# Performance work log

Measured on AMD Instinct MI355X. Metric: run time of the kernel, lower is better.

## Reference

```python
import jax, jax.numpy as jnp
import numpy as np

GROUPS = 32
EPS = 1e-5


def setup_inputs() -> dict:
    key = jax.random.key(0)
    ks = jax.random.split(key, 6)
    B, H, W, C = 2, 64, 64, 512
    wscale = 0.02  # keep logits in a sane range for softmax
    return {
        "x": jax.random.normal(ks[0], (B, H, W, C), dtype=jnp.float32),
        "gamma": jnp.ones((C,), jnp.float32),
        "beta": jnp.zeros((C,), jnp.float32),
        "wq": jax.random.normal(ks[1], (C, C), dtype=jnp.float32) * wscale,
        "bq": jnp.zeros((C,), jnp.float32),
        "wk": jax.random.normal(ks[2], (C, C), dtype=jnp.float32) * wscale,
        "bk": jnp.zeros((C,), jnp.float32),
        "wv": jax.random.normal(ks[3], (C, C), dtype=jnp.float32) * wscale,
        "bv": jnp.zeros((C,), jnp.float32),
        "wp": jax.random.normal(ks[4], (C, C), dtype=jnp.float32) * wscale,
        "bp": jnp.zeros((C,), jnp.float32),
    }


def _group_norm(x, gamma, beta):
    B, H, W, C = x.shape
    xg = x.reshape(B, H, W, GROUPS, C // GROUPS)
    mean = xg.mean(axis=(1, 2, 4), keepdims=True)
    var = xg.var(axis=(1, 2, 4), keepdims=True)
    xn = ((xg - mean) * jax.lax.rsqrt(var + EPS)).reshape(B, H, W, C)
    return xn * gamma + beta


def reference(x, gamma, beta, wq, bq, wk, bk, wv, bv, wp, bp):
    B, H, W, C = x.shape
    xn = _group_norm(x, gamma, beta)
    # 1x1 convs == per-pixel linear layers
    q = (xn @ wq + bq).reshape(B, H * W, C)
    k = (xn @ wk + bk).reshape(B, H * W, C)
    v = (xn @ wv + bv).reshape(B, H * W, C)
    scale = C ** (-0.5)
    attn = jax.nn.softmax(jnp.einsum("bqc,bkc->bqk", q, k) * scale, axis=-1)
    out = jnp.einsum("bqk,bkc->bqc", attn, v).reshape(B, H, W, C)
    return (out @ wp + bp) + x
```

## Files before the change

kernel.cpp:

```cpp
#include <hip/hip_runtime.h>


typedef __bf16 bf16_t;
typedef __bf16 bf16x8 __attribute__((ext_vector_type(8)));
typedef __bf16 bf16x4 __attribute__((ext_vector_type(4)));
typedef float  f32x4  __attribute__((ext_vector_type(4)));

__device__ __forceinline__ bf16x8 ld8(const bf16_t* p) {
    return *reinterpret_cast<const bf16x8*>(p);
}
__device__ __forceinline__ f32x4 mfma16(bf16x8 a, bf16x8 b, f32x4 c) {
    return __builtin_amdgcn_mfma_f32_16x16x32_bf16(a, b, c, 0, 0, 0);
}
__device__ __forceinline__ void gload16(const bf16_t* gp, bf16_t* lp) {
    __builtin_amdgcn_global_load_lds(
        (const __attribute__((address_space(1))) void*)gp,
        (__attribute__((address_space(3))) void*)lp, 16, 0, 0);
}

#define NPIX 8192
#define C512 512
#define SEQ  4096
#define QSCALE 0.044194173824159216f

__global__ __launch_bounds__(256) void gn_sum_k(const float* __restrict__ x,
                                                float* __restrict__ accum) {
    int bg    = blockIdx.x >> 3;
    int slice = blockIdx.x & 7;
    int b = bg >> 5, g = bg & 31;
    const float* xp = x + (size_t)b * SEQ * C512 + g * 16;
    float s = 0.f, s2 = 0.f;
    #pragma unroll
    for (int pp = 0; pp < 2; pp++) {
        int p = slice * 512 + pp * 256 + threadIdx.x;
        const float4* q = reinterpret_cast<const float4*>(xp + (size_t)p * C512);
        #pragma unroll
        for (int i = 0; i < 4; i++) {
            float4 v = q[i];
            s  += v.x + v.y + v.z + v.w;
            s2 += v.x*v.x + v.y*v.y + v.z*v.z + v.w*v.w;
        }
    }
    #pragma unroll
    for (int off = 32; off >= 1; off >>= 1) {
        s  += __shfl_down(s, off);
        s2 += __shfl_down(s2, off);
    }
    __shared__ float rs[4], rs2[4];
    int wave = threadIdx.x >> 6;
    if ((threadIdx.x & 63) == 0) { rs[wave] = s; rs2[wave] = s2; }
    __syncthreads();
    if (threadIdx.x == 0) {
        float S = rs[0] + rs[1] + rs[2] + rs[3];
        float S2 = rs2[0] + rs2[1] + rs2[2] + rs2[3];
        atomicAdd(&accum[bg * 2],     S);
        atomicAdd(&accum[bg * 2 + 1], S2);
    }
}

__global__ __launch_bounds__(256) void wt_conv_k(const float* wq, const float* wk,
                                                 const float* wv, const float* wp,
                                                 bf16_t* wqkvT, bf16_t* wpT) {
    int y = blockIdx.y;
    const float* w = (y == 0) ? wq : (y == 1) ? wk : (y == 2) ? wv : wp;
    float scale = (y == 0) ? QSCALE : 1.0f;
    int tid = blockIdx.x * 256 + threadIdx.x;
    int n = tid >> 9, k = tid & 511;
    bf16_t val = (bf16_t)(w[(size_t)k * C512 + n] * scale);
    if (y < 3) wqkvT[((size_t)y * C512 + n) * C512 + k] = val;
    else       wpT[(size_t)n * C512 + k] = val;
}

__global__ __launch_bounds__(256) void bias_merge_k(const float* bq, const float* bk,
                                                    const float* bv, float* bqkv) {
    int i = blockIdx.x * 256 + threadIdx.x;
    float v = (i < 512) ? bq[i] * QSCALE : (i < 1024) ? bk[i - 512] : bv[i - 1024];
    bqkv[i] = v;
}

__global__ __launch_bounds__(256) void xn_k(const float* __restrict__ x,
                                            const float* __restrict__ accum,
                                            const float* __restrict__ gamma,
                                            const float* __restrict__ beta,
                                            bf16_t* __restrict__ xn) {
    size_t idx = ((size_t)blockIdx.x * 256 + threadIdx.x) * 4;
    int c = (int)(idx & 511);
    size_t pix = idx >> 9;
    int b = (int)(pix >> 12);
    int g = c >> 4;
    float sum = accum[(b * 32 + g) * 2];
    float ssq = accum[(b * 32 + g) * 2 + 1];
    float mean = sum * (1.f / 65536.f);
    float var  = ssq * (1.f / 65536.f) - mean * mean;
    float rstd = rsqrtf(var + 1e-5f);
    float4 v  = *reinterpret_cast<const float4*>(x + idx);
    float4 gm = *reinterpret_cast<const float4*>(gamma + c);
    float4 bt = *reinterpret_cast<const float4*>(beta + c);
    bf16x4 o;
    o[0] = (bf16_t)((v.x - mean) * rstd * gm.x + bt.x);
    o[1] = (bf16_t)((v.y - mean) * rstd * gm.y + bt.y);
    o[2] = (bf16_t)((v.z - mean) * rstd * gm.z + bt.z);
    o[3] = (bf16_t)((v.w - mean) * rstd * gm.w + bt.w);
    *reinterpret_cast<bf16x4*>(xn + idx) = o;
}

template <int MODE>
__global__ __launch_bounds__(256, 2) void gemm128_k(
        const bf16_t* __restrict__ Aall, const bf16_t* __restrict__ Ball,
        const float* __restrict__ bias, const float* __restrict__ resid,
        void* __restrict__ out0, void* __restrict__ out1,
        void* __restrict__ out2, void* __restrict__ out3,
        float* __restrict__ lsum) {
    constexpr int TM  = (MODE == 3) ? 64 : 128;
    constexpr int ASZ = TM * 32;
    constexpr int ACH = TM / 16;
    constexpr int CPW = (ACH + 8) / 4;
    constexpr int MI  = TM / 32;
    __shared__ bf16_t smem[2 * ASZ + 8192];

    int lane = threadIdx.x & 63;
    int w    = threadIdx.x >> 6;
    int wr   = w >> 1, wc = w & 1;
    int lrow = lane & 15, quad = lane >> 4;

    const bf16_t* A = Aall;
    const bf16_t* B = Ball;
    size_t lda = 512, ldb = 512;
    int ksteps = 16;

    int bm = blockIdx.x * TM, bn = blockIdx.y * 128;

    auto stage = [&](int buf, int ks) {
        size_t k0 = (size_t)ks * 32;
        #pragma unroll
        for (int ii = 0; ii < CPW; ii++) {
            int c = w * CPW + ii;
            if (c < ACH) {
                const bf16_t* gpA = A + (size_t)(bm + c * 16 + lrow) * lda + k0 + quad * 8;
                gload16(gpA, &smem[buf * ASZ + c * 512]);
            } else {
                int cb = c - ACH;
                const bf16_t* gpB = B + (size_t)(bn + cb * 16 + lrow) * ldb + k0 + quad * 8;
                gload16(gpB, &smem[2 * ASZ + buf * 4096 + cb * 512]);
            }
        }
    };

    f32x4 acc[MI][4] = {};

    stage(0, 0);

    for (int ks = 0; ks < ksteps; ks++) {
        int cur = ks & 1;
        __syncthreads();
        if (ks + 1 < ksteps) stage(1 - cur, ks + 1);

        const bf16_t* al = &smem[cur * ASZ + (wr * MI) * 512];
        const bf16_t* bl = &smem[2 * ASZ + cur * 4096 + (wc * 4) * 512];
        bf16x8 af[MI], bf[4];
        #pragma unroll
        for (int m = 0; m < MI; m++) af[m] = ld8(al + m * 512 + lane * 8);
        #pragma unroll
        for (int n = 0; n < 4; n++) bf[n] = ld8(bl + n * 512 + lane * 8);
        #pragma unroll
        for (int m = 0; m < MI; m++)
            #pragma unroll
            for (int n = 0; n < 4; n++)
                acc[m][n] = mfma16(af[m], bf[n], acc[m][n]);
    }

    #pragma unroll
    for (int m = 0; m < MI; m++) {
        int rowb = bm + wr * (TM / 2) + m * 16 + quad * 4;
        #pragma unroll
        for (int n = 0; n < 4; n++) {
            int col = bn + wc * 64 + n * 16 + lrow;
            #pragma unroll
            for (int i = 0; i < 4; i++) {
                int row = rowb + i;
                float v = acc[m][n][i];
                if (MODE == 0) {
                    int seg = col >> 9, c = col & 511;
                    bf16_t val = (bf16_t)(v + bias[col]);
                    if (seg == 0) {
                        ((bf16_t*)out0)[(size_t)row * C512 + c] = val;
                    } else if (seg == 1) {
                        ((bf16_t*)out1)[(size_t)row * C512 + c] = val;
                    } else {
                        int b = row >> 12, s = row & 4095;
                        ((bf16_t*)out2)[((size_t)(b * C512 + c)) * SEQ + s] = val;
                    }
                } else {
                    size_t idx = (size_t)row * C512 + col;
                    ((float*)out0)[idx] = v + bias[col] + resid[idx];
                }
            }
        }
    }
}

__global__ __launch_bounds__(512, 1) void fattn_k(
        const bf16_t* __restrict__ Q, const bf16_t* __restrict__ K,
        const bf16_t* __restrict__ VT, bf16_t* __restrict__ Op0,
        bf16_t* __restrict__ Op1, float* __restrict__ lsum) {
    __shared__ bf16_t Kl[2][32 * 512];
    __shared__ bf16_t Vl[2][512 * 32];
    __shared__ bf16_t Pl[64 * 32];

    int bid = blockIdx.x;
    int xcd = bid & 7, loc = bid >> 3;
    int b   = (xcd >> 1) & 1;
    int kv  = xcd & 1;
    int q0  = ((xcd >> 2) * 32 + loc) * 64;
    int key0 = kv * 2048;

    const bf16_t* Qb = Q  + (size_t)b * SEQ * C512;
    const bf16_t* Kb = K  + (size_t)b * SEQ * C512;
    const bf16_t* Vb = VT + (size_t)b * C512 * SEQ;
    bf16_t* Op = kv ? Op1 : Op0;

    int lane = threadIdx.x & 63;
    int w    = threadIdx.x >> 6;
    int lrow = lane & 15, quad = lane >> 4;
    int qt = w & 3, kt = w >> 2;

    bf16x8 qf[16];
    const bf16_t* qp = Qb + (size_t)(q0 + qt * 16 + lrow) * C512 + quad * 8;
    #pragma unroll
    for (int ks = 0; ks < 16; ks++) qf[ks] = ld8(qp + ks * 32);

    auto stage = [&](int buf, int t) {
        #pragma unroll
        for (int ii = 0; ii < 8; ii++) {
            int cc = w * 8 + ii;
            if (cc < 32) {
                int ks = cc >> 1, ktc = cc & 1;
                const bf16_t* gp = Kb +
                    (size_t)(key0 + t * 32 + ktc * 16 + lrow) * C512 + ks * 32 + quad * 8;
                gload16(gp, &Kl[buf][cc * 512]);
            } else {
                int ct = cc - 32;
                const bf16_t* gp = Vb +
                    (size_t)(ct * 16 + lrow) * SEQ + key0 + t * 32 + quad * 8;
                gload16(gp, &Vl[buf][ct * 512]);
            }
        }
    };

    f32x4 oacc[4][4] = {};
    float rs[4] = {0.f, 0.f, 0.f, 0.f};

    stage(0, 0);

    for (int t = 0; t < 64; t++) {
        int cur = t & 1;
        __syncthreads();
        if (t < 63) stage(cur ^ 1, t + 1);

        f32x4 sa = {0.f, 0.f, 0.f, 0.f};
        #pragma unroll
        for (int ks = 0; ks < 16; ks++) {
            bf16x8 bf = ld8(&Kl[cur][(ks * 2 + kt) * 512 + lane * 8]);
            sa = mfma16(qf[ks], bf, sa);
        }
        #pragma unroll
        for (int i = 0; i < 4; i++) {
            float p = __expf(fminf(sa[i], 20.0f));
            rs[i] += p;
            int off = qt * 512 + (quad * 4 + i) * 8 +
                      (kt * 2 + (lrow >> 3)) * 128 + (lrow & 7);
            Pl[off] = (bf16_t)p;
        }
        asm volatile("s_waitcnt lgkmcnt(0)" ::: "memory");
        __builtin_amdgcn_s_barrier();
        __builtin_amdgcn_sched_barrier(0);

        bf16x8 pa[4];
        #pragma unroll
        for (int m = 0; m < 4; m++) pa[m] = ld8(&Pl[m * 512 + lane * 8]);
        #pragma unroll
        for (int n = 0; n < 4; n++) {
            bf16x8 vf = ld8(&Vl[cur][(w * 4 + n) * 512 + lane * 8]);
            #pragma unroll
            for (int m = 0; m < 4; m++)
                oacc[m][n] = mfma16(pa[m], vf, oacc[m][n]);
        }
    }

    #pragma unroll
    for (int i = 0; i < 4; i++) {
        float r = rs[i];
        r += __shfl_xor(r, 1);
        r += __shfl_xor(r, 2);
        r += __shfl_xor(r, 4);
        r += __shfl_xor(r, 8);
        if (lrow == 0)
            atomicAdd(&lsum[(size_t)b * SEQ + q0 + qt * 16 + quad * 4 + i], r);
    }

    #pragma unroll
    for (int m = 0; m < 4; m++) {
        int row = q0 + m * 16 + quad * 4;
        #pragma unroll
        for (int n = 0; n < 4; n++) {
            int col = w * 64 + n * 16 + lrow;
            #pragma unroll
            for (int i = 0; i < 4; i++)
                Op[((size_t)b * SEQ + row + i) * C512 + col] = (bf16_t)oacc[m][n][i];
        }
    }
}

__global__ __launch_bounds__(256) void attn_combine2_k(
        const bf16_t* __restrict__ Op0, const bf16_t* __restrict__ Op1,
        const float* __restrict__ lsum, bf16_t* __restrict__ O) {
    int idx = blockIdx.x * 256 + threadIdx.x;
    int row = idx >> 6;
    int c8  = (idx & 63) << 3;
    float inv = 1.0f / lsum[row];
    size_t base = (size_t)row * C512 + c8;
    bf16x8 o0 = ld8(Op0 + base), o1 = ld8(Op1 + base);
    bf16x8 o;
    #pragma unroll
    for (int j = 0; j < 8; j++)
        o[j] = (bf16_t)(((float)o0[j] + (float)o1[j]) * inv);
    *reinterpret_cast<bf16x8*>(O + base) = o;
}

extern "C" void kernel_launch(void* const* d_in, const int* in_sizes, int n_in,
                              void* d_out, int out_size, void* d_ws, size_t ws_size,
                              hipStream_t stream) {
    const float* x     = (const float*)d_in[0];
    const float* gamma = (const float*)d_in[1];
    const float* beta  = (const float*)d_in[2];
    const float* wq = (const float*)d_in[3];  const float* bq = (const float*)d_in[4];
    const float* wk = (const float*)d_in[5];  const float* bk = (const float*)d_in[6];
    const float* wv = (const float*)d_in[7];  const float* bv = (const float*)d_in[8];
    const float* wp = (const float*)d_in[9];  const float* bp = (const float*)d_in[10];
    float* out = (float*)d_out;

    char* ws = (char*)d_ws;
    size_t off = 0;
    float*  bqkv   = (float*)(ws + off);   off += 1536 * sizeof(float);
    float*  lsum   = (float*)(ws + off);   off += (size_t)NPIX * sizeof(float);
    float*  accum  = (float*)(ws + off);   off += 128 * sizeof(float);
    bf16_t* xn     = (bf16_t*)(ws + off);  off += (size_t)NPIX * C512 * 2;
    bf16_t* wqkvT  = (bf16_t*)(ws + off);  off += (size_t)3 * C512 * C512 * 2;
    bf16_t* wpT    = (bf16_t*)(ws + off);  off += (size_t)C512 * C512 * 2;
    bf16_t* Qb     = (bf16_t*)(ws + off);  off += (size_t)NPIX * C512 * 2;
    bf16_t* Kb     = (bf16_t*)(ws + off);  off += (size_t)NPIX * C512 * 2;
    bf16_t* VTb    = (bf16_t*)(ws + off);  off += (size_t)NPIX * C512 * 2;
    bf16_t* Op0    = (bf16_t*)(ws + off);  off += (size_t)NPIX * C512 * 2;
    bf16_t* Op1    = (bf16_t*)(ws + off);  off += (size_t)NPIX * C512 * 2;
    bf16_t* Ob  = xn;

    hipMemsetAsync(lsum, 0, (size_t)(NPIX + 128) * sizeof(float), stream);

    gn_sum_k<<<512, 256, 0, stream>>>(x, accum);
    wt_conv_k<<<dim3(1024, 4), 256, 0, stream>>>(wq, wk, wv, wp, wqkvT, wpT);
    bias_merge_k<<<6, 256, 0, stream>>>(bq, bk, bv, bqkv);
    xn_k<<<4096, 256, 0, stream>>>(x, accum, gamma, beta, xn);

    gemm128_k<0><<<dim3(64, 12, 1), 256, 0, stream>>>(
        xn, wqkvT, bqkv, nullptr, Qb, Kb, VTb, nullptr, nullptr);

    fattn_k<<<256, 512, 0, stream>>>(Qb, Kb, VTb, Op0, Op1, lsum);

    attn_combine2_k<<<2048, 256, 0, stream>>>(Op0, Op1, lsum, Ob);

    gemm128_k<3><<<dim3(128, 4, 1), 256, 0, stream>>>(
        Ob, wpT, bp, x, out, nullptr, nullptr, nullptr, nullptr);
}
```

Before: 305.3 us.

## Warp-specialize attention: QK/softmax waves feed PV waves via double-buffered P

Splits the eight waves of the flash-attention block into two roles. Four waves compute QK^T and exp for 64 queries and write P into a double-buffered LDS tile. The other four waves load V and run the PV MFMAs one key tile behind. The aim is to overlap the score phase with the value phase instead of serializing them behind a barrier on every tile. In exchange, each wave now holds more accumulator registers (32 f32x4 on the PV side), and the pipeline needs one extra iteration to drain.

```diff
diff --git a/kernel.cpp b/kernel.cpp
--- a/kernel.cpp
+++ b/kernel.cpp
@@ -204,8 +204,8 @@
         const bf16_t* __restrict__ VT, bf16_t* __restrict__ Op0,
         bf16_t* __restrict__ Op1, float* __restrict__ lsum) {
     __shared__ bf16_t Kl[2][32 * 512];
-    __shared__ bf16_t Vl[2][512 * 32];
-    __shared__ bf16_t Pl[64 * 32];
+    __shared__ bf16_t Vl[2][32 * 512];
+    __shared__ bf16_t Pl[2][64 * 32];
 
     int bid = blockIdx.x;
     int xcd = bid & 7, loc = bid >> 3;
@@ -222,91 +222,117 @@
     int lane = threadIdx.x & 63;
     int w    = threadIdx.x >> 6;
     int lrow = lane & 15, quad = lane >> 4;
-    int qt = w & 3, kt = w >> 2;
-
-    bf16x8 qf[16];
-    const bf16_t* qp = Qb + (size_t)(q0 + qt * 16 + lrow) * C512 + quad * 8;
-    #pragma unroll
-    for (int ks = 0; ks < 16; ks++) qf[ks] = ld8(qp + ks * 32);
-
-    auto stage = [&](int buf, int t) {
-        #pragma unroll
-        for (int ii = 0; ii < 8; ii++) {
-            int cc = w * 8 + ii;
-            if (cc < 32) {
-                int ks = cc >> 1, ktc = cc & 1;
-                const bf16_t* gp = Kb +
-                    (size_t)(key0 + t * 32 + ktc * 16 + lrow) * C512 + ks * 32 + quad * 8;
-                gload16(gp, &Kl[buf][cc * 512]);
-            } else {
-                int ct = cc - 32;
-                const bf16_t* gp = Vb +
-                    (size_t)(ct * 16 + lrow) * SEQ + key0 + t * 32 + quad * 8;
-                gload16(gp, &Vl[buf][ct * 512]);
-            }
-        }
-    };
-
-    f32x4 oacc[4][4] = {};
-    float rs[4] = {0.f, 0.f, 0.f, 0.f};
-
-    stage(0, 0);
-
-    for (int t = 0; t < 64; t++) {
-        int cur = t & 1;
-        __syncthreads();
-        if (t < 63) stage(cur ^ 1, t + 1);
-
-        f32x4 sa = {0.f, 0.f, 0.f, 0.f};
-        #pragma unroll
-        for (int ks = 0; ks < 16; ks++) {
-            bf16x8 bf = ld8(&Kl[cur][(ks * 2 + kt) * 512 + lane * 8]);
-            sa = mfma16(qf[ks], bf, sa);
-        }
-        #pragma unroll
-        for (int i = 0; i < 4; i++) {
-            float p = __expf(fminf(sa[i], 20.0f));
-            rs[i] += p;
-            int off = qt * 512 + (quad * 4 + i) * 8 +
-                      (kt * 2 + (lrow >> 3)) * 128 + (lrow & 7);
-            Pl[off] = (bf16_t)p;
-        }
-        asm volatile("s_waitcnt lgkmcnt(0)" ::: "memory");
-        __builtin_amdgcn_s_barrier();
-        __builtin_amdgcn_sched_barrier(0);
-
-        bf16x8 pa[4];
-        #pragma unroll
-        for (int m = 0; m < 4; m++) pa[m] = ld8(&Pl[m * 512 + lane * 8]);
-        #pragma unroll
-        for (int n = 0; n < 4; n++) {
-            bf16x8 vf = ld8(&Vl[cur][(w * 4 + n) * 512 + lane * 8]);
-            #pragma unroll
-            for (int m = 0; m < 4; m++)
-                oacc[m][n] = mfma16(pa[m], vf, oacc[m][n]);
-        }
-    }
-
-    #pragma unroll
-    for (int i = 0; i < 4; i++) {
-        float r = rs[i];
-        r += __shfl_xor(r, 1);
-        r += __shfl_xor(r, 2);
-        r += __shfl_xor(r, 4);
-        r += __shfl_xor(r, 8);
-        if (lrow == 0)
-            atomicAdd(&lsum[(size_t)b * SEQ + q0 + qt * 16 + quad * 4 + i], r);
-    }
-
-    #pragma unroll
-    for (int m = 0; m < 4; m++) {
-        int row = q0 + m * 16 + quad * 4;
-        #pragma unroll
-        for (int n = 0; n < 4; n++) {
-            int col = w * 64 + n * 16 + lrow;
-            #pragma unroll
-            for (int i = 0; i < 4; i++)
-                Op[((size_t)b * SEQ + row + i) * C512 + col] = (bf16_t)oacc[m][n][i];
+
+    #pragma unroll
+    for (int ii = 0; ii < 4; ii++) {
+        int cc = w * 4 + ii;
+        int ks = cc >> 1, ktc = cc & 1;
+        const bf16_t* gp = Kb + (size_t)(key0 + ktc * 16 + lrow) * C512 + ks * 32 + quad * 8;
+        gload16(gp, &Kl[0][cc * 512]);
+    }
+    __syncthreads();
+
+    if (w < 4) {
+        int qh = w >> 1, kt = w & 1;
+        bf16x8 qf[2][16];
+        const bf16_t* qp = Qb + (size_t)(q0 + qh * 32 + lrow) * C512 + quad * 8;
+        #pragma unroll
+        for (int m = 0; m < 2; m++)
+            #pragma unroll
+            for (int ks = 0; ks < 16; ks++)
+                qf[m][ks] = ld8(qp + (size_t)m * 16 * C512 + ks * 32);
+        float rs[2][4] = {};
+
+        for (int i = 0; i <= 64; ++i) {
+            int cur = i & 1;
+            if (i < 64) {
+                if (i < 63) {
+                    #pragma unroll
+                    for (int ii = 0; ii < 8; ii++) {
+                        int cc = w * 8 + ii;
+                        int ks = cc >> 1, ktc = cc & 1;
+                        const bf16_t* gp = Kb +
+                            (size_t)(key0 + (i + 1) * 32 + ktc * 16 + lrow) * C512 +
+                            ks * 32 + quad * 8;
+                        gload16(gp, &Kl[cur ^ 1][cc * 512]);
+                    }
+                }
+                f32x4 sacc0 = {}, sacc1 = {};
+                #pragma unroll
+                for (int ks = 0; ks < 16; ks++) {
+                    bf16x8 kf = ld8(&Kl[cur][(ks * 2 + kt) * 512 + lane * 8]);
+                    sacc0 = mfma16(qf[0][ks], kf, sacc0);
+                    sacc1 = mfma16(qf[1][ks], kf, sacc1);
+                }
+                #pragma unroll
+                for (int i4 = 0; i4 < 4; i4++) {
+                    float p0 = __expf(fminf(sacc0[i4], 20.0f));
+                    float p1 = __expf(fminf(sacc1[i4], 20.0f));
+                    rs[0][i4] += p0;
+                    rs[1][i4] += p1;
+                    int obase = (quad * 4 + i4) * 8 +
+                                (kt * 2 + (lrow >> 3)) * 128 + (lrow & 7);
+                    Pl[cur][(qh * 2 + 0) * 512 + obase] = (bf16_t)p0;
+                    Pl[cur][(qh * 2 + 1) * 512 + obase] = (bf16_t)p1;
+                }
+            }
+            __syncthreads();
+        }
+        #pragma unroll
+        for (int m = 0; m < 2; m++) {
+            #pragma unroll
+            for (int i4 = 0; i4 < 4; i4++) {
+                float r = rs[m][i4];
+                r += __shfl_xor(r, 1);
+                r += __shfl_xor(r, 2);
+                r += __shfl_xor(r, 4);
+                r += __shfl_xor(r, 8);
+                if (lrow == 0)
+                    atomicAdd(&lsum[(size_t)b * SEQ + q0 + qh * 32 + m * 16 +
+                                    quad * 4 + i4], r);
+            }
+        }
+    } else {
+        int u = w - 4;
+        f32x4 acc[4][8] = {};
+        for (int i = 0; i <= 64; ++i) {
+            int cur = i & 1;
+            if (i < 64) {
+                #pragma unroll
+                for (int ii = 0; ii < 8; ii++) {
+                    int ct = u * 8 + ii;
+                    const bf16_t* gp = Vb + (size_t)(ct * 16 + lrow) * SEQ +
+                                       key0 + i * 32 + quad * 8;
+                    gload16(gp, &Vl[cur][ct * 512]);
+                }
+            }
+            if (i >= 1) {
+                int pb = cur ^ 1;
+                bf16x8 pa[4];
+                #pragma unroll
+                for (int mm = 0; mm < 4; mm++)
+                    pa[mm] = ld8(&Pl[pb][mm * 512 + lane * 8]);
+                #pragma unroll
+                for (int n = 0; n < 8; n++) {
+                    bf16x8 vf = ld8(&Vl[pb][(u * 8 + n) * 512 + lane * 8]);
+                    #pragma unroll
+                    for (int mm = 0; mm < 4; mm++)
+                        acc[mm][n] = mfma16(pa[mm], vf, acc[mm][n]);
+                }
+            }
+            __syncthreads();
+        }
+        #pragma unroll
+        for (int mm = 0; mm < 4; mm++) {
+            int row = q0 + mm * 16 + quad * 4;
+            #pragma unroll
+            for (int n = 0; n < 8; n++) {
+                int col = u * 128 + n * 16 + lrow;
+                #pragma unroll
+                for (int i4 = 0; i4 < 4; i4++)
+                    Op[((size_t)b * SEQ + row + i4) * C512 + col] =
+                        (bf16_t)acc[mm][n][i4];
+            }
         }
     }
 }
```

Result: slower. 320.0 us (+4.8%).

## Software-pipeline attention loop: overlap PV of previous tile with QK of current

Applied to the files above, without the earlier changes.

Restructures the flash-attention main loop so each iteration computes the P·V product for the previous key tile while computing QK scores and exp for the current tile. P is double-buffered and V staging is decoupled from K staging, with V loaded one iteration later. This drops the mid-iteration barrier and leaves one barrier per iteration. The QK accumulation is also split into two independent MFMA chains to shorten the dependency chain. The cost is an extra P buffer, one extra loop iteration, and V loads that have less lead time before use.

```diff
diff --git a/kernel.cpp b/kernel.cpp
--- a/kernel.cpp
+++ b/kernel.cpp
@@ -204,8 +204,8 @@
         const bf16_t* __restrict__ VT, bf16_t* __restrict__ Op0,
         bf16_t* __restrict__ Op1, float* __restrict__ lsum) {
     __shared__ bf16_t Kl[2][32 * 512];
-    __shared__ bf16_t Vl[2][512 * 32];
-    __shared__ bf16_t Pl[64 * 32];
+    __shared__ bf16_t Vl[2][32 * 512];
+    __shared__ bf16_t Pl[2][64 * 32];
 
     int bid = blockIdx.x;
     int xcd = bid & 7, loc = bid >> 3;
@@ -229,62 +229,72 @@
     #pragma unroll
     for (int ks = 0; ks < 16; ks++) qf[ks] = ld8(qp + ks * 32);
 
-    auto stage = [&](int buf, int t) {
-        #pragma unroll
-        for (int ii = 0; ii < 8; ii++) {
-            int cc = w * 8 + ii;
-            if (cc < 32) {
-                int ks = cc >> 1, ktc = cc & 1;
-                const bf16_t* gp = Kb +
-                    (size_t)(key0 + t * 32 + ktc * 16 + lrow) * C512 + ks * 32 + quad * 8;
-                gload16(gp, &Kl[buf][cc * 512]);
-            } else {
-                int ct = cc - 32;
-                const bf16_t* gp = Vb +
-                    (size_t)(ct * 16 + lrow) * SEQ + key0 + t * 32 + quad * 8;
-                gload16(gp, &Vl[buf][ct * 512]);
-            }
+    auto stageK = [&](int buf, int t) {
+        #pragma unroll
+        for (int ii = 0; ii < 4; ii++) {
+            int cc = w * 4 + ii;
+            int ks = cc >> 1, ktc = cc & 1;
+            const bf16_t* gp = Kb +
+                (size_t)(key0 + t * 32 + ktc * 16 + lrow) * C512 + ks * 32 + quad * 8;
+            gload16(gp, &Kl[buf][cc * 512]);
+        }
+    };
+    auto stageV = [&](int buf, int t) {
+        #pragma unroll
+        for (int ii = 0; ii < 4; ii++) {
+            int ct = w * 4 + ii;
+            const bf16_t* gp = Vb + (size_t)(ct * 16 + lrow) * SEQ +
+                               key0 + t * 32 + quad * 8;
+            gload16(gp, &Vl[buf][ct * 512]);
         }
     };
 
     f32x4 oacc[4][4] = {};
     float rs[4] = {0.f, 0.f, 0.f, 0.f};
 
-    stage(0, 0);
-
-    for (int t = 0; t < 64; t++) {
+    stageK(0, 0);
+    __syncthreads();
+
+    for (int t = 0; t <= 64; ++t) {
         int cur = t & 1;
+        if (t < 64) {
+            if (t < 63) stageK(cur ^ 1, t + 1);
+            stageV(cur, t);
+        }
+        if (t >= 1) {
+            int pb = cur ^ 1;
+            bf16x8 pa[4];
+            #pragma unroll
+            for (int mm = 0; mm < 4; mm++)
+                pa[mm] = ld8(&Pl[pb][mm * 512 + lane * 8]);
+            #pragma unroll
+            for (int n = 0; n < 4; n++) {
+                bf16x8 vf = ld8(&Vl[pb][(w * 4 + n) * 512 + lane * 8]);
+                #pragma unroll
+                for (int mm = 0; mm < 4; mm++)
+                    oacc[mm][n] = mfma16(pa[mm], vf, oacc[mm][n]);
+            }
+        }
+        if (t < 64) {
+            f32x4 sa0 = {}, sa1 = {};
+            #pragma unroll
+            for (int ks = 0; ks < 8; ks++) {
+                bf16x8 kf0 = ld8(&Kl[cur][((2 * ks) * 2 + kt) * 512 + lane * 8]);
+                bf16x8 kf1 = ld8(&Kl[cur][((2 * ks + 1) * 2 + kt) * 512 + lane * 8]);
+                sa0 = mfma16(qf[2 * ks],     kf0, sa0);
+                sa1 = mfma16(qf[2 * ks + 1], kf1, sa1);
+            }
+            f32x4 sa = sa0 + sa1;
+            #pragma unroll
+            for (int i4 = 0; i4 < 4; i4++) {
+                float p = __expf(fminf(sa[i4], 20.0f));
+                rs[i4] += p;
+                int off = qt * 512 + (quad * 4 + i4) * 8 +
+                          (kt * 2 + (lrow >> 3)) * 128 + (lrow & 7);
+                Pl[cur][off] = (bf16_t)p;
+            }
+        }
         __syncthreads();
-        if (t < 63) stage(cur ^ 1, t + 1);
-
-        f32x4 sa = {0.f, 0.f, 0.f, 0.f};
-        #pragma unroll
-        for (int ks = 0; ks < 16; ks++) {
-            bf16x8 bf = ld8(&Kl[cur][(ks * 2 + kt) * 512 + lane * 8]);
-            sa = mfma16(qf[ks], bf, sa);
-        }
-        #pragma unroll
-        for (int i = 0; i < 4; i++) {
-            float p = __expf(fminf(sa[i], 20.0f));
-            rs[i] += p;
-            int off = qt * 512 + (quad * 4 + i) * 8 +
-                      (kt * 2 + (lrow >> 3)) * 128 + (lrow & 7);
-            Pl[off] = (bf16_t)p;
-        }
-        asm volatile("s_waitcnt lgkmcnt(0)" ::: "memory");
-        __builtin_amdgcn_s_barrier();
-        __builtin_amdgcn_sched_barrier(0);
-
-        bf16x8 pa[4];
-        #pragma unroll
-        for (int m = 0; m < 4; m++) pa[m] = ld8(&Pl[m * 512 + lane * 8]);
-        #pragma unroll
-        for (int n = 0; n < 4; n++) {
-            bf16x8 vf = ld8(&Vl[cur][(w * 4 + n) * 512 + lane * 8]);
-            #pragma unroll
-            for (int m = 0; m < 4; m++)
-                oacc[m][n] = mfma16(pa[m], vf, oacc[m][n]);
-        }
     }
 
     #pragma unroll
```

Result: slower. 332.5 us (+8.9%).

## Load V fragments directly from global memory into registers, dropping LDS staging

Applied to the files above, without the earlier changes.

V tiles are no longer staged through shared memory with async global-to-LDS loads. Each wave now loads its own V fragments straight from global memory into registers at the start of each iteration, which halves LDS use and staging work. The QK dot product is split into two independent accumulator chains, and the MFMA sections are wrapped in s_setprio to favour matrix issue. The risk is that global-load latency for V is exposed within the same iteration rather than being prefetched one step ahead.

```diff
diff --git a/kernel.cpp b/kernel.cpp
--- a/kernel.cpp
+++ b/kernel.cpp
@@ -204,7 +204,6 @@
         const bf16_t* __restrict__ VT, bf16_t* __restrict__ Op0,
         bf16_t* __restrict__ Op1, float* __restrict__ lsum) {
     __shared__ bf16_t Kl[2][32 * 512];
-    __shared__ bf16_t Vl[2][512 * 32];
     __shared__ bf16_t Pl[64 * 32];
 
     int bid = blockIdx.x;
@@ -229,40 +228,44 @@
     #pragma unroll
     for (int ks = 0; ks < 16; ks++) qf[ks] = ld8(qp + ks * 32);
 
-    auto stage = [&](int buf, int t) {
-        #pragma unroll
-        for (int ii = 0; ii < 8; ii++) {
-            int cc = w * 8 + ii;
-            if (cc < 32) {
-                int ks = cc >> 1, ktc = cc & 1;
-                const bf16_t* gp = Kb +
-                    (size_t)(key0 + t * 32 + ktc * 16 + lrow) * C512 + ks * 32 + quad * 8;
-                gload16(gp, &Kl[buf][cc * 512]);
-            } else {
-                int ct = cc - 32;
-                const bf16_t* gp = Vb +
-                    (size_t)(ct * 16 + lrow) * SEQ + key0 + t * 32 + quad * 8;
-                gload16(gp, &Vl[buf][ct * 512]);
-            }
+    auto stageK = [&](int buf, int t) {
+        #pragma unroll
+        for (int ii = 0; ii < 4; ii++) {
+            int cc = w * 4 + ii;
+            int ks = cc >> 1, ktc = cc & 1;
+            const bf16_t* gp = Kb +
+                (size_t)(key0 + t * 32 + ktc * 16 + lrow) * C512 + ks * 32 + quad * 8;
+            gload16(gp, &Kl[buf][cc * 512]);
         }
     };
+    const bf16_t* vbase = Vb + (size_t)(w * 64 + lrow) * SEQ + key0 + quad * 8;
 
     f32x4 oacc[4][4] = {};
     float rs[4] = {0.f, 0.f, 0.f, 0.f};
 
-    stage(0, 0);
+    stageK(0, 0);
 
     for (int t = 0; t < 64; t++) {
         int cur = t & 1;
         __syncthreads();
-        if (t < 63) stage(cur ^ 1, t + 1);
-
-        f32x4 sa = {0.f, 0.f, 0.f, 0.f};
-        #pragma unroll
-        for (int ks = 0; ks < 16; ks++) {
-            bf16x8 bf = ld8(&Kl[cur][(ks * 2 + kt) * 512 + lane * 8]);
-            sa = mfma16(qf[ks], bf, sa);
-        }
+        if (t < 63) stageK(1 - cur, t + 1);
+
+        bf16x8 vf[4];
+        const bf16_t* vp = vbase + (size_t)t * 32;
+        #pragma unroll
+        for (int n = 0; n < 4; n++) vf[n] = ld8(vp + (size_t)(n * 16) * SEQ);
+
+        f32x4 sa0 = {}, sa1 = {};
+        __builtin_amdgcn_s_setprio(1);
+        #pragma unroll
+        for (int ks = 0; ks < 8; ks++) {
+            bf16x8 kf0 = ld8(&Kl[cur][((2 * ks) * 2 + kt) * 512 + lane * 8]);
+            bf16x8 kf1 = ld8(&Kl[cur][((2 * ks + 1) * 2 + kt) * 512 + lane * 8]);
+            sa0 = mfma16(qf[2 * ks],     kf0, sa0);
+            sa1 = mfma16(qf[2 * ks + 1], kf1, sa1);
+        }
+        __builtin_amdgcn_s_setprio(0);
+        f32x4 sa = sa0 + sa1;
         #pragma unroll
         for (int i = 0; i < 4; i++) {
             float p = __expf(fminf(sa[i], 20.0f));
@@ -278,13 +281,13 @@
         bf16x8 pa[4];
         #pragma unroll
         for (int m = 0; m < 4; m++) pa[m] = ld8(&Pl[m * 512 + lane * 8]);
-        #pragma unroll
-        for (int n = 0; n < 4; n++) {
-            bf16x8 vf = ld8(&Vl[cur][(w * 4 + n) * 512 + lane * 8]);
+        __builtin_amdgcn_s_setprio(1);
+        #pragma unroll
+        for (int n = 0; n < 4; n++)
             #pragma unroll
             for (int m = 0; m < 4; m++)
-                oacc[m][n] = mfma16(pa[m], vf, oacc[m][n]);
-        }
+                oacc[m][n] = mfma16(pa[m], vf[n], oacc[m][n]);
+        __builtin_amdgcn_s_setprio(0);
     }
 
     #pragma unroll
```

New measurement: 341.1 us. 1.12x slower.
